# Optimization experiments

Measured on AMD Instinct MI355X. Metric: run time of the kernel, lower is better.

## Reference

```python
import jax, jax.numpy as jnp
import numpy as np

DROPOUT_P = 0.5

def _gcn_conv(h, W, b, src, dst, norm, self_norm, n):
    # h: [N, Din] -> [N, Dout]; symmetric-normalized aggregation with self loops
    h = h @ W
    msg = h[src] * norm[:, None]                       # [E, Dout]
    agg = jax.ops.segment_sum(msg, dst, num_segments=n)
    return agg + h * self_norm[:, None] + b


def setup_inputs() -> dict:
    key = jax.random.key(0)
    ks = jax.random.split(key, 8)
    N, E, D_IN, D_OUT = 50000, 800000, 512, 256
    H = 2 * D_OUT  # 512
    x = jax.random.normal(ks[0], (N, D_IN), dtype=jnp.float32)
    edge_index = jax.random.randint(ks[1], (2, E), 0, N, dtype=jnp.int64)
    s = 1.0 / np.sqrt(D_IN)
    W1 = jax.random.uniform(ks[2], (D_IN, H), jnp.float32, -s, s)
    b1 = jnp.zeros((H,), jnp.float32)
    s2 = 1.0 / np.sqrt(H)
    Wmu = jax.random.uniform(ks[3], (H, D_OUT), jnp.float32, -s2, s2)
    bmu = jnp.zeros((D_OUT,), jnp.float32)
    Wls = jax.random.uniform(ks[4], (H, D_OUT), jnp.float32, -s2, s2)
    bls = jnp.zeros((D_OUT,), jnp.float32)
    return {"x": x, "edge_index": edge_index, "W1": W1, "b1": b1,
            "Wmu": Wmu, "bmu": bmu, "Wls": Wls, "bls": bls}


def reference(x, edge_index, W1, b1, Wmu, bmu, Wls, bls):
    n = x.shape[0]
    src, dst = edge_index[0], edge_index[1]
    # GCN symmetric normalization with self loops: deg includes +1 self loop
    deg = jax.ops.segment_sum(jnp.ones_like(dst, dtype=x.dtype), dst, num_segments=n) + 1.0
    dinv = jax.lax.rsqrt(deg)
    norm = dinv[src] * dinv[dst]     # per-edge norm
    self_norm = dinv * dinv          # self-loop norm = 1/deg
    # dropout (train mode, deterministic mask)
    keep = jax.random.bernoulli(jax.random.key(42), 1.0 - DROPOUT_P, x.shape)
    h = jnp.where(keep, x / (1.0 - DROPOUT_P), 0.0)
    h = jax.nn.relu(_gcn_conv(h, W1, b1, src, dst, norm, self_norm, n))
    mu = _gcn_conv(h, Wmu, bmu, src, dst, norm, self_norm, n)
    logstd = _gcn_conv(h, Wls, bls, src, dst, norm, self_norm, n)
    return (mu, logstd)
```

## Files before the change

### kernel.cpp

```cpp
#include <hip/hip_runtime.h>
#include <hip/hip_bf16.h>

typedef __hip_bfloat16 bf16;
typedef __attribute__((ext_vector_type(8))) short short8;
typedef __attribute__((ext_vector_type(4))) float f32x4;

__device__ __forceinline__ float bfu(unsigned short b) {
    unsigned u = ((unsigned)b) << 16;
    float f;
    __builtin_memcpy(&f, &u, 4);
    return f;
}
__device__ __forceinline__ unsigned short f2b(float f) {
    return (unsigned short)(__hip_bfloat16_raw(__float2bfloat16(f)).x);
}

__device__ __forceinline__ void gl_lds16(const void* g, void* l) {
    __builtin_amdgcn_global_load_lds(
        (const __attribute__((address_space(1))) void*)g,
        (__attribute__((address_space(3))) void*)l, 16, 0, 0);
}

__device__ __forceinline__ bool keep_elem(unsigned idx) {
    const unsigned k0 = 0u, k1 = 42u;
    const unsigned k2 = k0 ^ k1 ^ 0x1BD11BDAu;
    unsigned x0 = k0;
    unsigned x1 = idx + k1;
#define TF_QR(R) { x0 += x1; x1 = (x1 << R) | (x1 >> (32 - R)); x1 ^= x0; }
    TF_QR(13) TF_QR(15) TF_QR(26) TF_QR(6)
    x0 += k1; x1 += k2 + 1u;
    TF_QR(17) TF_QR(29) TF_QR(16) TF_QR(24)
    x0 += k2; x1 += k0 + 2u;
    TF_QR(13) TF_QR(15) TF_QR(26) TF_QR(6)
    x0 += k0; x1 += k1 + 3u;
    TF_QR(17) TF_QR(29) TF_QR(16) TF_QR(24)
    x0 += k1; x1 += k2 + 4u;
    TF_QR(13) TF_QR(15) TF_QR(26) TF_QR(6)
    x0 += k2; x1 += k0 + 5u;
#undef TF_QR
    return (((x0 ^ x1) >> 31) & 1u) == 0u;
}

__global__ void detect_all_k(const unsigned* __restrict__ ei,
                             const unsigned short* __restrict__ x,
                             const unsigned short* __restrict__ w1,
                             int* __restrict__ flag) {
    __shared__ int red[256];
    if (blockIdx.x == 0) {
        unsigned v = 0;
        for (int i = threadIdx.x; i < 2048; i += 256) v |= ei[2 * i + 1];
        red[threadIdx.x] = (int)v;
        __syncthreads();
        for (int s = 128; s > 0; s >>= 1) {
            if (threadIdx.x < s) red[threadIdx.x] |= red[threadIdx.x + s];
            __syncthreads();
        }
        if (threadIdx.x == 0) flag[0] = (red[0] == 0) ? 1 : 0;
    } else {
        const unsigned short* p = (blockIdx.x == 1) ? x : w1;
        int cnt = 0;
        for (int i = threadIdx.x; i < 1024; i += 256) {
            unsigned short b = p[2 * i];
            int e = (b >> 7) & 0xFF;
            if ((b & 0x7FFF) == 0 || (e >= 100 && e < 140)) cnt++;
        }
        red[threadIdx.x] = cnt;
        __syncthreads();
        for (int s = 128; s > 0; s >>= 1) {
            if (threadIdx.x < s) red[threadIdx.x] += red[threadIdx.x + s];
            __syncthreads();
        }
        if (threadIdx.x == 0) flag[blockIdx.x] = (red[0] < 614) ? 1 : 0;
    }
}

__global__ void convert_edges_k(const void* __restrict__ src, int* __restrict__ out,
                                int twoE, const int* __restrict__ flag) {
    int i = blockIdx.x * 256 + threadIdx.x;
    if (i >= twoE) return;
    if (flag[0]) out[i] = (int)((const unsigned long long*)src)[i];
    else         out[i] = ((const int*)src)[i];
}

__global__ void canon_transpose_k(const void* __restrict__ src, unsigned short* __restrict__ dst,
                                  int K, int Nn, const int* __restrict__ flag, int fidx) {
    __shared__ unsigned short tile[16][17];
    int k0 = blockIdx.x * 16, n0 = blockIdx.y * 16;
    int k = k0 + threadIdx.y, n = n0 + threadIdx.x;
    unsigned short v;
    if (flag[fidx]) v = f2b(((const float*)src)[(size_t)k * Nn + n]);
    else            v = ((const unsigned short*)src)[(size_t)k * Nn + n];
    tile[threadIdx.y][threadIdx.x] = v;
    __syncthreads();
    int nn = n0 + threadIdx.y, kk = k0 + threadIdx.x;
    dst[(size_t)nn * K + kk] = tile[threadIdx.x][threadIdx.y];
}

__global__ void canon_bias_k(const void* __restrict__ b1, const void* __restrict__ bmu,
                             const void* __restrict__ bls, bf16* __restrict__ b1c,
                             bf16* __restrict__ bcat, int H, int DOUT,
                             const int* __restrict__ flag) {
    int i = blockIdx.x * 256 + threadIdx.x;
    int f = flag[2];
    if (i < H) {
        b1c[i] = f ? __float2bfloat16(((const float*)b1)[i]) : ((const bf16*)b1)[i];
    } else if (i < H + DOUT) {
        int j = i - H;
        bcat[j] = f ? __float2bfloat16(((const float*)bmu)[j]) : ((const bf16*)bmu)[j];
    } else if (i < H + 2 * DOUT) {
        int j = i - H - DOUT;
        bcat[DOUT + j] = f ? __float2bfloat16(((const float*)bls)[j]) : ((const bf16*)bls)[j];
    }
}

__global__ void zero_int_k(int* __restrict__ p, int n) {
    int i = blockIdx.x * 256 + threadIdx.x;
    if (i < n) p[i] = 0;
}
__global__ void deg_count_k(const int* __restrict__ edges, int* __restrict__ degi,
                            int E, int n) {
    int e = blockIdx.x * 256 + threadIdx.x;
    if (e >= E) return;
    int d = edges[E + e];
    d = (d < 0) ? 0 : (d >= n ? n - 1 : d);
    atomicAdd(&degi[d], 1);
}
__global__ void block_sums_k(const int* __restrict__ deg, int* __restrict__ partial, int n) {
    __shared__ int sh[256];
    int i = blockIdx.x * 256 + threadIdx.x;
    sh[threadIdx.x] = (i < n) ? deg[i] : 0;
    __syncthreads();
    for (int s = 128; s > 0; s >>= 1) {
        if (threadIdx.x < s) sh[threadIdx.x] += sh[threadIdx.x + s];
        __syncthreads();
    }
    if (threadIdx.x == 0) partial[blockIdx.x] = sh[0];
}
__global__ void scan_partials_k(int* __restrict__ partial, int G) {
    __shared__ int sh[256];
    int v = (threadIdx.x < G) ? partial[threadIdx.x] : 0;
    sh[threadIdx.x] = v;
    __syncthreads();
    for (int s = 1; s < 256; s <<= 1) {
        int t = 0;
        if (threadIdx.x >= s) t = sh[threadIdx.x - s];
        __syncthreads();
        sh[threadIdx.x] += t;
        __syncthreads();
    }
    if (threadIdx.x < G) partial[threadIdx.x] = sh[threadIdx.x] - v;
}
__global__ void scan_block_k(const int* __restrict__ deg, const int* __restrict__ partial,
                             int* __restrict__ row_ptr, float* __restrict__ dinv, int n) {
    __shared__ int sh[256];
    int i = blockIdx.x * 256 + threadIdx.x;
    int v = (i < n) ? deg[i] : 0;
    sh[threadIdx.x] = v;
    __syncthreads();
    for (int s = 1; s < 256; s <<= 1) {
        int t = 0;
        if (threadIdx.x >= s) t = sh[threadIdx.x - s];
        __syncthreads();
        sh[threadIdx.x] += t;
        __syncthreads();
    }
    int incl = sh[threadIdx.x];
    int base = partial[blockIdx.x];
    if (i < n) {
        row_ptr[i] = base + incl - v;
        dinv[i] = rsqrtf(1.0f + (float)v);
    }
    if (i == n - 1) row_ptr[n] = base + incl;
}
__global__ void fill_k(const int* __restrict__ edges, const int* __restrict__ row_ptr,
                       int* __restrict__ cnt, int* __restrict__ col, int E, int n) {
    int e = blockIdx.x * 256 + threadIdx.x;
    if (e >= E) return;
    int s = edges[e], d = edges[E + e];
    s = (s < 0) ? 0 : (s >= n ? n - 1 : s);
    d = (d < 0) ? 0 : (d >= n ? n - 1 : d);
    int pos = row_ptr[d] + atomicAdd(&cnt[d], 1);
    col[pos] = s;
}

__global__ __launch_bounds__(512) void gemm_wide_k(
    const void* __restrict__ Ain, const bf16* __restrict__ Bt,
    bf16* __restrict__ Cb, float* __restrict__ Cf, float* __restrict__ Cf2,
    const bf16* __restrict__ bias, int M, int K,
    const int* __restrict__ flag, int drop) {
    __shared__ short sA[128 * 32];
    __shared__ short sB[512 * 32];
    const int tid = threadIdx.x;
    const int lane = tid & 63;
    const int w = tid >> 6;
    const int m0 = blockIdx.x * 128;
    const int wm = (w & 1) * 64;
    const int wn = (w >> 1) * 128;

    f32x4 acc[4][8] = {};

    const int arow = tid >> 2;
    const int acol = (tid & 3) * 8;
    int grow = m0 + arow;
    if (grow >= M) grow = M - 1;
    const bool xf32 = drop && flag[1];

    for (int kk = 0; kk < K; kk += 32) {
#pragma unroll
        for (int q = 0; q < 4; ++q)
            gl_lds16(Bt + (size_t)(q * 128 + arow) * K + kk + acol,
                     &sB[q * 4096 + tid * 8]);
        if (!drop) {
            gl_lds16((const bf16*)Ain + (size_t)grow * K + kk + acol, &sA[tid * 8]);
        } else {
            unsigned gidx = (unsigned)grow * (unsigned)K + (unsigned)(kk + acol);
            float v[8];
            if (xf32) {
                const f32x4* p = (const f32x4*)Ain;
                f32x4 a = p[gidx >> 2], b = p[(gidx >> 2) + 1];
#pragma unroll
                for (int k2 = 0; k2 < 4; ++k2) { v[k2] = a[k2]; v[4 + k2] = b[k2]; }
            } else {
                short8 u = ((const short8*)Ain)[gidx >> 3];
#pragma unroll
                for (int k2 = 0; k2 < 8; ++k2) v[k2] = bfu((unsigned short)u[k2]);
            }
            short8 o;
#pragma unroll
            for (int k2 = 0; k2 < 8; ++k2) {
                float f = keep_elem(gidx + k2) ? v[k2] * 2.0f : 0.0f;
                o[k2] = (short)f2b(f);
            }
            *(short8*)&sA[tid * 8] = o;
        }
        __syncthreads();

        const int fr = lane & 15;
        const int fk = (lane >> 4) * 8;
        short8 af[4], bfr2[8];
#pragma unroll
        for (int i = 0; i < 4; ++i)
            af[i] = *(const short8*)&sA[(wm + i * 16 + fr) * 32 + fk];
#pragma unroll
        for (int j = 0; j < 8; ++j)
            bfr2[j] = *(const short8*)&sB[(wn + j * 16 + fr) * 32 + fk];
#pragma unroll
        for (int i = 0; i < 4; ++i)
#pragma unroll
            for (int j = 0; j < 8; ++j)
                acc[i][j] = __builtin_amdgcn_mfma_f32_16x16x32_bf16(
                    af[i], bfr2[j], acc[i][j], 0, 0, 0);
        __syncthreads();
    }

    const int crow = (lane >> 4) * 4;
    const int ccol = lane & 15;
    if (Cf) {
        const int side = (wn >= 256) ? 1 : 0;
        float* base = side ? Cf2 : Cf;
        const int nb = wn - side * 256;
#pragma unroll
        for (int i = 0; i < 4; ++i) {
#pragma unroll
            for (int r = 0; r < 4; ++r) {
                int row = m0 + wm + i * 16 + crow + r;
                if (row >= M) continue;
                float* cp = base + (size_t)row * 256 + nb;
#pragma unroll
                for (int j = 0; j < 8; ++j) {
                    int c = j * 16 + ccol;
                    cp[c] = acc[i][j][r] + __bfloat162float(bias[wn + c]);
                }
            }
        }
    } else {
#pragma unroll
        for (int i = 0; i < 4; ++i) {
#pragma unroll
            for (int r = 0; r < 4; ++r) {
                int row = m0 + wm + i * 16 + crow + r;
                if (row >= M) continue;
                bf16* cp = Cb + (size_t)row * 512 + wn;
#pragma unroll
                for (int j = 0; j < 8; ++j)
                    cp[j * 16 + ccol] = __float2bfloat16(acc[i][j][r]);
            }
        }
    }
}

__global__ __launch_bounds__(256) void gather_k(
    const bf16* __restrict__ t, const int* __restrict__ row_ptr,
    const int* __restrict__ col, const float* __restrict__ dinv,
    const bf16* __restrict__ bias, bf16* __restrict__ outp, int mode, int N) {
    const int node = blockIdx.x * 4 + (threadIdx.x >> 6);
    if (node >= N) return;
    const int lane = threadIdx.x & 63;
    const short8* tp = (const short8*)t;
    const int beg = row_ptr[node];
    const int end = row_ptr[node + 1];
    const float dv = dinv[node];
    float acc[8] = {0.f, 0.f, 0.f, 0.f, 0.f, 0.f, 0.f, 0.f};

    int e = beg;
    const int elim = beg + ((end - beg) & ~7);
    if (e < elim) {
        int c[8];
        float w[8];
#pragma unroll
        for (int k = 0; k < 8; ++k) c[k] = col[e + k];
#pragma unroll
        for (int k = 0; k < 8; ++k) w[k] = dinv[c[k]] * dv;
        for (;;) {
            short8 u[8];
#pragma unroll
            for (int k = 0; k < 8; ++k) u[k] = tp[(size_t)c[k] * 64 + lane];
            const int en = e + 8;
            const bool more = en < elim;
            int cn[8];
            float wn2[8];
            if (more) {
#pragma unroll
                for (int k = 0; k < 8; ++k) cn[k] = col[en + k];
#pragma unroll
                for (int k = 0; k < 8; ++k) wn2[k] = dinv[cn[k]] * dv;
            }
#pragma unroll
            for (int k = 0; k < 8; ++k) {
                const float wk = w[k];
#pragma unroll
                for (int j = 0; j < 8; ++j)
                    acc[j] += wk * bfu((unsigned short)u[k][j]);
            }
            e = en;
            if (!more) break;
#pragma unroll
            for (int k = 0; k < 8; ++k) { c[k] = cn[k]; w[k] = wn2[k]; }
        }
    }
    for (; e + 4 <= end; e += 4) {
        int s0 = col[e + 0], s1 = col[e + 1], s2 = col[e + 2], s3 = col[e + 3];
        float w0 = dinv[s0] * dv, w1 = dinv[s1] * dv;
        float w2 = dinv[s2] * dv, w3 = dinv[s3] * dv;
        short8 u0 = tp[(size_t)s0 * 64 + lane];
        short8 u1 = tp[(size_t)s1 * 64 + lane];
        short8 u2 = tp[(size_t)s2 * 64 + lane];
        short8 u3 = tp[(size_t)s3 * 64 + lane];
#pragma unroll
        for (int k = 0; k < 8; ++k) {
            acc[k] += w0 * bfu((unsigned short)u0[k]);
            acc[k] += w1 * bfu((unsigned short)u1[k]);
            acc[k] += w2 * bfu((unsigned short)u2[k]);
            acc[k] += w3 * bfu((unsigned short)u3[k]);
        }
    }
    for (; e < end; ++e) {
        int s = col[e];
        float w = dinv[s] * dv;
        short8 u = tp[(size_t)s * 64 + lane];
#pragma unroll
        for (int k = 0; k < 8; ++k) acc[k] += w * bfu((unsigned short)u[k]);
    }
    {
        short8 u = tp[(size_t)node * 64 + lane];
        float w = dv * dv;
#pragma unroll
        for (int k = 0; k < 8; ++k) acc[k] += w * bfu((unsigned short)u[k]);
    }
    if (mode == 1) {
        short8 bs = ((const short8*)bias)[lane];
#pragma unroll
        for (int k = 0; k < 8; ++k) {
            acc[k] += bfu((unsigned short)bs[k]);
            acc[k] = fmaxf(acc[k], 0.f);
        }
    }
    short8 o;
#pragma unroll
    for (int k = 0; k < 8; ++k) o[k] = (short)f2b(acc[k]);
    ((short8*)outp)[(size_t)node * 64 + lane] = o;
}

extern "C" void kernel_launch(void* const* d_in, const int* in_sizes, int n_in,
                              void* d_out, int out_size, void* d_ws, size_t ws_size,
                              hipStream_t stream) {
    const void* xin   = d_in[0];
    const void* ei    = d_in[1];
    const void* W1in  = d_in[2];
    const void* b1in  = d_in[3];
    const void* Wmuin = d_in[4];
    const void* bmuin = d_in[5];
    const void* Wlsin = d_in[6];
    const void* blsin = d_in[7];
    float* out = (float*)d_out;

    const int H    = in_sizes[3];
    const int DOUT = in_sizes[5];
    const int DIN  = in_sizes[2] / H;
    const int N    = in_sizes[0] / DIN;
    const int E    = in_sizes[1] / 2;
    const int G    = (N + 255) / 256;

    char* ws = (char*)d_ws;
    size_t off = 0;
    auto alloc = [&](size_t bytes) {
        void* p = ws + off;
        off = (off + bytes + 255) & ~(size_t)255;
        return p;
    };
    int*   flag    = (int*)alloc(256);
    int*   edges   = (int*)alloc((size_t)2 * E * 4);
    int*   degcnt  = (int*)alloc((size_t)2 * N * 4);
    int*   degi    = degcnt;
    int*   cnt     = degcnt + N;
    int*   row_ptr = (int*)alloc((size_t)(N + 1) * 4);
    int*   partial = (int*)alloc((size_t)G * 4);
    int*   col     = (int*)alloc((size_t)E * 4);
    float* dinv    = (float*)alloc((size_t)N * 4);
    bf16*  t1      = (bf16*)alloc((size_t)N * H * 2);
    bf16*  g1      = (bf16*)alloc((size_t)N * H * 2);
    bf16*  h1      = (bf16*)alloc((size_t)N * H * 2);
    bf16*  W1t     = (bf16*)alloc((size_t)DIN * H * 2);
    bf16*  Wcat    = (bf16*)alloc((size_t)H * 2 * DOUT * 2);
    bf16*  b1c     = (bf16*)alloc((size_t)H * 2);
    bf16*  bcat    = (bf16*)alloc((size_t)2 * DOUT * 2);
    if (off > ws_size) return;

    const int twoE = 2 * E;
    hipLaunchKernelGGL(detect_all_k, dim3(3), dim3(256), 0, stream,
                       (const unsigned*)ei, (const unsigned short*)xin,
                       (const unsigned short*)W1in, flag);

    hipLaunchKernelGGL(convert_edges_k, dim3((twoE + 255) / 256), dim3(256), 0, stream,
                       ei, edges, twoE, flag);
    hipLaunchKernelGGL(canon_transpose_k, dim3(DIN / 16, H / 16), dim3(16, 16), 0, stream,
                       W1in, (unsigned short*)W1t, DIN, H, flag, 2);
    hipLaunchKernelGGL(canon_transpose_k, dim3(H / 16, DOUT / 16), dim3(16, 16), 0, stream,
                       Wmuin, (unsigned short*)Wcat, H, DOUT, flag, 2);
    hipLaunchKernelGGL(canon_transpose_k, dim3(H / 16, DOUT / 16), dim3(16, 16), 0, stream,
                       Wlsin, (unsigned short*)(Wcat + (size_t)DOUT * H), H, DOUT, flag, 2);
    hipLaunchKernelGGL(canon_bias_k, dim3((H + 2 * DOUT + 255) / 256), dim3(256), 0, stream,
                       b1in, bmuin, blsin, b1c, bcat, H, DOUT, flag);

    hipLaunchKernelGGL(zero_int_k, dim3((2 * N + 255) / 256), dim3(256), 0, stream, degcnt, 2 * N);
    hipLaunchKernelGGL(deg_count_k, dim3((E + 255) / 256), dim3(256), 0, stream, edges, degi, E, N);
    hipLaunchKernelGGL(block_sums_k, dim3(G), dim3(256), 0, stream, degi, partial, N);
    hipLaunchKernelGGL(scan_partials_k, dim3(1), dim3(256), 0, stream, partial, G);
    hipLaunchKernelGGL(scan_block_k, dim3(G), dim3(256), 0, stream, degi, partial, row_ptr, dinv, N);
    hipLaunchKernelGGL(fill_k, dim3((E + 255) / 256), dim3(256), 0, stream, edges, row_ptr, cnt, col, E, N);

    hipLaunchKernelGGL(gemm_wide_k, dim3((N + 127) / 128), dim3(512), 0, stream,
                       xin, W1t, t1, (float*)nullptr, (float*)nullptr,
                       (const bf16*)nullptr, N, DIN, flag, 1);
    hipLaunchKernelGGL(gather_k, dim3((N + 3) / 4), dim3(256), 0, stream,
                       t1, row_ptr, col, dinv, b1c, h1, 1, N);

    hipLaunchKernelGGL(gather_k, dim3((N + 3) / 4), dim3(256), 0, stream,
                       h1, row_ptr, col, dinv, (const bf16*)nullptr, g1, 0, N);
    hipLaunchKernelGGL(gemm_wide_k, dim3((N + 127) / 128), dim3(512), 0, stream,
                       g1, Wcat, (bf16*)nullptr, out, out + (size_t)N * DOUT,
                       bcat, N, H, flag, 0);
}
```

Baseline: 668.2 us.

## Double GEMM K-tile to 64 with XOR-swizzled LDS layout

The wide GEMM kernel now stages 64-wide K slices per iteration instead of 32, halving the number of barrier pairs and loop trips. Each thread loads multiple 16-byte chunks per row, and LDS chunk positions are XOR-swizzled by row to avoid bank conflicts on the fragment reads. This raises LDS use to about 80KB per block, which may lower occupancy.

```diff
diff --git a/kernel.cpp b/kernel.cpp
--- a/kernel.cpp
+++ b/kernel.cpp
@@ -188,8 +188,8 @@
     bf16* __restrict__ Cb, float* __restrict__ Cf, float* __restrict__ Cf2,
     const bf16* __restrict__ bias, int M, int K,
     const int* __restrict__ flag, int drop) {
-    __shared__ short sA[128 * 32];
-    __shared__ short sB[512 * 32];
+    __shared__ short sA[128 * 64];
+    __shared__ short sB[512 * 64];
     const int tid = threadIdx.x;
     const int lane = tid & 63;
     const int w = tid >> 6;
@@ -199,57 +199,73 @@
 
     f32x4 acc[4][8] = {};
 
-    const int arow = tid >> 2;
-    const int acol = (tid & 3) * 8;
-    int grow = m0 + arow;
-    if (grow >= M) grow = M - 1;
+    const int srow = tid >> 3;
+    const int schunk = (tid & 7) ^ (srow & 7);
+    const int scol = schunk * 8;
     const bool xf32 = drop && flag[1];
 
-    for (int kk = 0; kk < K; kk += 32) {
-#pragma unroll
-        for (int q = 0; q < 4; ++q)
-            gl_lds16(Bt + (size_t)(q * 128 + arow) * K + kk + acol,
-                     &sB[q * 4096 + tid * 8]);
+    for (int kk = 0; kk < K; kk += 64) {
+#pragma unroll
+        for (int p = 0; p < 8; ++p)
+            gl_lds16(Bt + (size_t)(p * 64 + srow) * K + kk + scol,
+                     &sB[p * 4096 + tid * 8]);
         if (!drop) {
-            gl_lds16((const bf16*)Ain + (size_t)grow * K + kk + acol, &sA[tid * 8]);
+#pragma unroll
+            for (int p = 0; p < 2; ++p) {
+                int r = m0 + p * 64 + srow; if (r >= M) r = M - 1;
+                gl_lds16((const bf16*)Ain + (size_t)r * K + kk + scol,
+                         &sA[p * 4096 + tid * 8]);
+            }
         } else {
-            unsigned gidx = (unsigned)grow * (unsigned)K + (unsigned)(kk + acol);
-            float v[8];
-            if (xf32) {
-                const f32x4* p = (const f32x4*)Ain;
-                f32x4 a = p[gidx >> 2], b = p[(gidx >> 2) + 1];
-#pragma unroll
-                for (int k2 = 0; k2 < 4; ++k2) { v[k2] = a[k2]; v[4 + k2] = b[k2]; }
-            } else {
-                short8 u = ((const short8*)Ain)[gidx >> 3];
-#pragma unroll
-                for (int k2 = 0; k2 < 8; ++k2) v[k2] = bfu((unsigned short)u[k2]);
-            }
-            short8 o;
-#pragma unroll
-            for (int k2 = 0; k2 < 8; ++k2) {
-                float f = keep_elem(gidx + k2) ? v[k2] * 2.0f : 0.0f;
-                o[k2] = (short)f2b(f);
-            }
-            *(short8*)&sA[tid * 8] = o;
+#pragma unroll
+            for (int p = 0; p < 2; ++p) {
+                int r = m0 + p * 64 + srow; if (r >= M) r = M - 1;
+                unsigned gidx = (unsigned)r * (unsigned)K + (unsigned)(kk + scol);
+                float v[8];
+                if (xf32) {
+                    const f32x4* pp = (const f32x4*)Ain;
+                    f32x4 a = pp[gidx >> 2], b = pp[(gidx >> 2) + 1];
+#pragma unroll
+                    for (int k2 = 0; k2 < 4; ++k2) { v[k2] = a[k2]; v[4 + k2] = b[k2]; }
+                } else {
+                    short8 u = ((const short8*)Ain)[gidx >> 3];
+#pragma unroll
+                    for (int k2 = 0; k2 < 8; ++k2) v[k2] = bfu((unsigned short)u[k2]);
+                }
+                short8 o;
+#pragma unroll
+                for (int k2 = 0; k2 < 8; ++k2) {
+                    float f = keep_elem(gidx + k2) ? v[k2] * 2.0f : 0.0f;
+                    o[k2] = (short)f2b(f);
+                }
+                *(short8*)&sA[p * 4096 + tid * 8] = o;
+            }
         }
         __syncthreads();
 
         const int fr = lane & 15;
-        const int fk = (lane >> 4) * 8;
-        short8 af[4], bfr2[8];
-#pragma unroll
-        for (int i = 0; i < 4; ++i)
-            af[i] = *(const short8*)&sA[(wm + i * 16 + fr) * 32 + fk];
-#pragma unroll
-        for (int j = 0; j < 8; ++j)
-            bfr2[j] = *(const short8*)&sB[(wn + j * 16 + fr) * 32 + fk];
-#pragma unroll
-        for (int i = 0; i < 4; ++i)
-#pragma unroll
-            for (int j = 0; j < 8; ++j)
-                acc[i][j] = __builtin_amdgcn_mfma_f32_16x16x32_bf16(
-                    af[i], bfr2[j], acc[i][j], 0, 0, 0);
+        const int q = lane >> 4;
+#pragma unroll
+        for (int ks = 0; ks < 2; ++ks) {
+            const int slot = ks * 4 + q;
+            short8 af[4], bf2[8];
+#pragma unroll
+            for (int i = 0; i < 4; ++i) {
+                int r = wm + i * 16 + fr;
+                af[i] = *(const short8*)&sA[r * 64 + ((slot ^ (r & 7)) * 8)];
+            }
+#pragma unroll
+            for (int j = 0; j < 8; ++j) {
+                int r = wn + j * 16 + fr;
+                bf2[j] = *(const short8*)&sB[r * 64 + ((slot ^ (r & 7)) * 8)];
+            }
+#pragma unroll
+            for (int i = 0; i < 4; ++i)
+#pragma unroll
+                for (int j = 0; j < 8; ++j)
+                    acc[i][j] = __builtin_amdgcn_mfma_f32_16x16x32_bf16(
+                        af[i], bf2[j], acc[i][j], 0, 0, 0);
+        }
         __syncthreads();
     }
 
```

Result: faster. 643.2 us (-3.7%).
